# Kernel optimization log

Hardware: AMD Instinct MI355X
Metric: run time of the kernel (lower is better)

## Reference

```python
import jax, jax.numpy as jnp
import numpy as np

B, S, H = 16, 8192, 256


def setup_inputs() -> dict:
    key = jax.random.key(0)
    k1, k2, k3, k4, k5, k6 = jax.random.split(key, 6)
    # He/Glorot-ish scaling for the linear layer is irrelevant for correctness; use small randn.
    return {
        "query": jax.random.normal(k1, (B, 1, H), dtype=jnp.float32),
        "key": jax.random.normal(k2, (B, S, H), dtype=jnp.float32),
        "value": jax.random.normal(k3, (B, S, H), dtype=jnp.float32),
        "W_attn": jax.random.normal(k4, (H, 2 * H), dtype=jnp.float32) * 0.05,  # nn.Linear(2H, H).weight
        "b_attn": jax.random.normal(k5, (H,), dtype=jnp.float32) * 0.05,
        "v": jax.random.uniform(k6, (H,), dtype=jnp.float32),  # torch.rand init
    }


def reference(query, key, value, W_attn, b_attn, v):
    # Faithful to: tanh(Linear(cat([query.repeat(S), key], -1))) @ v -> softmax -> weighted sum.
    # Split the Linear weight so we never materialize the repeated/concatenated [B,S,2H] tensor:
    # cat([q,k]) @ W.T == q @ Wq.T + k @ Wk.T, with Wq = W[:, :H], Wk = W[:, H:].
    Wq = W_attn[:, :H]  # [H, H]
    Wk = W_attn[:, H:]  # [H, H]
    hidden = jnp.tanh(
        jnp.einsum("bqh,oh->bqo", query, Wq)        # [B,1,H], broadcasts over S
        + jnp.einsum("bsh,oh->bso", key, Wk)        # [B,S,H]
        + b_attn
    )  # [B,S,H]
    scores = jnp.einsum("bsh,h->bs", hidden, v)      # [B,S]
    attn_weights = jax.nn.softmax(scores, axis=-1)   # softmax over sequence
    context = jnp.einsum("bs,bsh->bh", attn_weights, value)[:, None, :]  # [B,1,H]
    return context, attn_weights
```

## Files before the change

kernel.cpp:

```cpp
#include <hip/hip_runtime.h>

#define B_SZ 16
#define S_SZ 8192
#define H_SZ 256

typedef _Float16 half8 __attribute__((ext_vector_type(8)));
typedef float f32x4 __attribute__((ext_vector_type(4)));

__device__ __forceinline__ float tanh_fast(float x) {
  float e = __expf(2.0f * x);
  return 1.0f - 2.0f / (e + 1.0f);
}

__global__ __launch_bounds__(256) void prep_kernel(
    const float* __restrict__ query, const float* __restrict__ W_attn,
    const float* __restrict__ b_attn, float* __restrict__ qb) {
  const int b = blockIdx.x;
  const int jo = blockIdx.y;
  const int wid = threadIdx.x >> 6;
  const int lane = threadIdx.x & 63;
  const float4 q4 = *(const float4*)(query + b * H_SZ + lane * 4);
#pragma unroll 4
  for (int i = 0; i < 16; i++) {
    const int o = jo * 64 + wid * 16 + i;
    const float4 w = *(const float4*)(W_attn + (size_t)o * 512 + lane * 4);
    float p = q4.x * w.x + q4.y * w.y + q4.z * w.z + q4.w * w.w;
#pragma unroll
    for (int off = 32; off >= 1; off >>= 1) p += __shfl_xor(p, off, 64);
    if (lane == 0) qb[b * H_SZ + o] = p + b_attn[o];
  }
}

__global__ __launch_bounds__(1024, 4) void fused_kernel(
    const float* __restrict__ key, const float* __restrict__ value,
    const float* __restrict__ W_attn, const float* __restrict__ qb,
    const float* __restrict__ vvec, float* __restrict__ scores,
    float* __restrict__ ctxp, float* __restrict__ mblk,
    float* __restrict__ zblk) {
  __shared__ _Float16 kbuf[2][32 * 256];
  __shared__ float psum[2][32];
  __shared__ float warr[32];
  __shared__ float msh;
  __shared__ float zsh;
  __shared__ float ssh;
  __shared__ float4 comb[16][64];

  const int tid = threadIdx.x;
  const int wid = tid >> 6;
  const int lane = tid & 63;
  const int n = lane & 15;
  const int quad = lane >> 4;
  const int rowBase = blockIdx.x * 256;
  const int b = rowBase >> 13;

  half8 afrag[8];
  {
    const float* wrow = W_attn + (size_t)(wid * 16 + n) * 512 + 256 + quad * 8;
#pragma unroll
    for (int ks = 0; ks < 8; ks++) {
      float4 f0 = *(const float4*)(wrow + ks * 32);
      float4 f1 = *(const float4*)(wrow + ks * 32 + 4);
      half8 a;
      a[0] = (_Float16)f0.x; a[1] = (_Float16)f0.y;
      a[2] = (_Float16)f0.z; a[3] = (_Float16)f0.w;
      a[4] = (_Float16)f1.x; a[5] = (_Float16)f1.y;
      a[6] = (_Float16)f1.z; a[7] = (_Float16)f1.w;
      afrag[ks] = a;
    }
  }
  float qbv[4], vvv[4];
#pragma unroll
  for (int rg = 0; rg < 4; rg++) {
    qbv[rg] = qb[b * H_SZ + wid * 16 + quad * 4 + rg];
    vvv[rg] = vvec[wid * 16 + quad * 4 + rg];
  }

  if (tid < 64) ((float*)psum)[tid] = 0.f;
  if (tid == 0) {
    msh = -1e30f;
    zsh = 0.f;
  }

  const int srow = tid >> 5;
  const int sseg = tid & 31;
  const size_t sbase = (size_t)(rowBase + srow) * H_SZ + sseg * 8;
  const int sdst = srow * 256 + ((sseg ^ srow) << 3);

  const float* vbase = value + (size_t)(rowBase + 2 * wid) * H_SZ + lane * 4;

  {
    float4 f0 = *(const float4*)(key + sbase);
    float4 f1 = *(const float4*)(key + sbase + 4);
    half8 h;
    h[0] = (_Float16)f0.x; h[1] = (_Float16)f0.y;
    h[2] = (_Float16)f0.z; h[3] = (_Float16)f0.w;
    h[4] = (_Float16)f1.x; h[5] = (_Float16)f1.y;
    h[6] = (_Float16)f1.z; h[7] = (_Float16)f1.w;
    *(half8*)&kbuf[0][sdst] = h;
  }
  __syncthreads();

  float4 acc4 = {0.f, 0.f, 0.f, 0.f};

  for (int c = 0; c < 8; c++) {
    const float4 va = *(const float4*)(vbase + (size_t)c * 32 * H_SZ);
    const float4 vb = *(const float4*)(vbase + (size_t)c * 32 * H_SZ + H_SZ);
    float4 g0, g1;
    if (c < 7) {
      const size_t nb = sbase + (size_t)(c + 1) * 32 * H_SZ;
      g0 = *(const float4*)(key + nb);
      g1 = *(const float4*)(key + nb + 4);
    }
    const _Float16* kb = kbuf[c & 1];
#pragma unroll
    for (int rt = 0; rt < 2; rt++) {
      const int lrow = rt * 16 + n;
      f32x4 acc = {0.f, 0.f, 0.f, 0.f};
#pragma unroll
      for (int ks = 0; ks < 8; ks++) {
        half8 bfrag =
            *(const half8*)&kb[lrow * 256 + (((ks * 4 + quad) ^ lrow) << 3)];
        acc = __builtin_amdgcn_mfma_f32_16x16x32_f16(afrag[ks], bfrag, acc,
                                                     0, 0, 0);
      }
      float p = 0.f;
#pragma unroll
      for (int rg = 0; rg < 4; rg++)
        p = fmaf(vvv[rg], tanh_fast(qbv[rg] + acc[rg]), p);
      p += __shfl_xor(p, 16, 64);
      p += __shfl_xor(p, 32, 64);
      if (quad == 0) atomicAdd(&psum[c & 1][lrow], p);
    }
    if (c < 7) {
      half8 h;
      h[0] = (_Float16)g0.x; h[1] = (_Float16)g0.y;
      h[2] = (_Float16)g0.z; h[3] = (_Float16)g0.w;
      h[4] = (_Float16)g1.x; h[5] = (_Float16)g1.y;
      h[6] = (_Float16)g1.z; h[7] = (_Float16)g1.w;
      *(half8*)&kbuf[(c + 1) & 1][sdst] = h;
    }
    __syncthreads();

    if (wid == 0) {
      float s = (lane < 32) ? psum[c & 1][lane] : -1e30f;
      if (lane < 32) {
        scores[rowBase + c * 32 + lane] = s;
        psum[c & 1][lane] = 0.f;
      }
      float cm = s;
#pragma unroll
      for (int off = 32; off >= 1; off >>= 1)
        cm = fmaxf(cm, __shfl_xor(cm, off, 64));
      const float m_old = msh;
      const float m_new = fmaxf(m_old, cm);
      const float scl = __expf(m_old - m_new);
      float w = (lane < 32) ? __expf(s - m_new) : 0.f;
      if (lane < 32) warr[lane] = w;
      float zc = w;
#pragma unroll
      for (int off = 32; off >= 1; off >>= 1) zc += __shfl_xor(zc, off, 64);
      if (lane == 0) {
        msh = m_new;
        zsh = fmaf(zsh, scl, zc);
        ssh = scl;
      }
    }
    __syncthreads();

    const float scl = ssh;
    const float w0 = warr[2 * wid];
    const float w1 = warr[2 * wid + 1];
    acc4.x = fmaf(w1, vb.x, fmaf(w0, va.x, acc4.x * scl));
    acc4.y = fmaf(w1, vb.y, fmaf(w0, va.y, acc4.y * scl));
    acc4.z = fmaf(w1, vb.z, fmaf(w0, va.z, acc4.z * scl));
    acc4.w = fmaf(w1, vb.w, fmaf(w0, va.w, acc4.w * scl));
  }

  comb[wid][lane] = acc4;
  __syncthreads();
  if (tid < 64) {
    float4 t4 = comb[0][tid];
#pragma unroll
    for (int j = 1; j < 16; j++) {
      const float4 u = comb[j][tid];
      t4.x += u.x; t4.y += u.y; t4.z += u.z; t4.w += u.w;
    }
    *(float4*)(ctxp + (size_t)blockIdx.x * 256 + tid * 4) = t4;
  }
  if (tid == 0) {
    mblk[blockIdx.x] = msh;
    zblk[blockIdx.x] = zsh;
  }
}

__global__ __launch_bounds__(1024) void combine_kernel(
    const float* __restrict__ ctxp, const float* __restrict__ mblk,
    const float* __restrict__ zblk, float* __restrict__ attn,
    float* __restrict__ ctx) {
  const int b = blockIdx.x;
  const int t = threadIdx.x;
  __shared__ float ms[32], zs[32];
  if (t < 32) {
    ms[t] = mblk[b * 32 + t];
    zs[t] = zblk[b * 32 + t];
  }
  __syncthreads();
  float m = -1e30f;
#pragma unroll
  for (int j = 0; j < 32; j++) m = fmaxf(m, ms[j]);
  float Z = 0.f;
  float e[32];
#pragma unroll
  for (int j = 0; j < 32; j++) {
    e[j] = __expf(ms[j] - m);
    Z = fmaf(zs[j], e[j], Z);
  }
  const float invZ = 1.0f / Z;
  if (t < 256) {
    float acc = 0.f;
#pragma unroll
    for (int j = 0; j < 32; j++)
      acc = fmaf(ctxp[(size_t)(b * 32 + j) * 256 + t], e[j], acc);
    ctx[b * H_SZ + t] = acc * invZ;
  }
  float* arow = attn + (size_t)b * S_SZ;
#pragma unroll
  for (int k = 0; k < 8; k++) {
    const int idx = k * 1024 + t;
    arow[idx] = __expf(arow[idx] - m) * invZ;
  }
}

extern "C" void kernel_launch(void* const* d_in, const int* in_sizes, int n_in,
                              void* d_out, int out_size, void* d_ws,
                              size_t ws_size, hipStream_t stream) {
  const float* query = (const float*)d_in[0];
  const float* key = (const float*)d_in[1];
  const float* value = (const float*)d_in[2];
  const float* W_attn = (const float*)d_in[3];
  const float* b_attn = (const float*)d_in[4];
  const float* vvec = (const float*)d_in[5];

  float* out = (float*)d_out;
  float* ctx = out;
  float* attn = out + 4096;
  float* ctxp = (float*)d_ws;
  float* mblk = ctxp + 512 * 256;
  float* zblk = mblk + 512;

  prep_kernel<<<dim3(B_SZ, 4), 256, 0, stream>>>(query, W_attn, b_attn, ctx);
  fused_kernel<<<512, 1024, 0, stream>>>(key, value, W_attn, ctx, vvec, attn,
                                         ctxp, mblk, zblk);
  combine_kernel<<<B_SZ, 1024, 0, stream>>>(ctxp, mblk, zblk, attn, ctx);
}
```

Baseline: 313.5 us.

## Halve block size, give each warp two output tiles, and do softmax redundantly per warp

The fused kernel now runs 512 threads per block instead of 1024. Each warp computes two 16-wide output tiles with two MFMA accumulators and reuses each B fragment read from shared memory. The online-softmax update, previously done by warp 0 and broadcast through shared memory behind a second barrier, is now computed redundantly in every warp using shuffles, which removes one __syncthreads per chunk. The psum buffer gets one slot per chunk so it never needs resetting. In exchange, each thread holds twice the A fragments and does twice the key/value loads, which raises register pressure and may reduce how many waves can be resident.

```diff
diff --git a/kernel.cpp b/kernel.cpp
--- a/kernel.cpp
+++ b/kernel.cpp
@@ -31,19 +31,15 @@
   }
 }
 
-__global__ __launch_bounds__(1024, 4) void fused_kernel(
+__global__ __launch_bounds__(512, 4) void fused_kernel(
     const float* __restrict__ key, const float* __restrict__ value,
     const float* __restrict__ W_attn, const float* __restrict__ qb,
     const float* __restrict__ vvec, float* __restrict__ scores,
     float* __restrict__ ctxp, float* __restrict__ mblk,
     float* __restrict__ zblk) {
   __shared__ _Float16 kbuf[2][32 * 256];
-  __shared__ float psum[2][32];
-  __shared__ float warr[32];
-  __shared__ float msh;
-  __shared__ float zsh;
-  __shared__ float ssh;
-  __shared__ float4 comb[16][64];
+  __shared__ float psum[8][32];
+  __shared__ float4 comb[8][64];
 
   const int tid = threadIdx.x;
   const int wid = tid >> 6;
@@ -51,11 +47,13 @@
   const int n = lane & 15;
   const int quad = lane >> 4;
   const int rowBase = blockIdx.x * 256;
-  const int b = rowBase >> 13;
-
-  half8 afrag[8];
-  {
-    const float* wrow = W_attn + (size_t)(wid * 16 + n) * 512 + 256 + quad * 8;
+  const int b = blockIdx.x >> 5;
+
+  half8 afrag[2][8];
+#pragma unroll
+  for (int ot = 0; ot < 2; ot++) {
+    const float* wrow =
+        W_attn + (size_t)((wid * 2 + ot) * 16 + n) * 512 + 256 + quad * 8;
 #pragma unroll
     for (int ks = 0; ks < 8; ks++) {
       float4 f0 = *(const float4*)(wrow + ks * 32);
@@ -65,115 +63,135 @@
       a[2] = (_Float16)f0.z; a[3] = (_Float16)f0.w;
       a[4] = (_Float16)f1.x; a[5] = (_Float16)f1.y;
       a[6] = (_Float16)f1.z; a[7] = (_Float16)f1.w;
-      afrag[ks] = a;
-    }
-  }
-  float qbv[4], vvv[4];
-#pragma unroll
-  for (int rg = 0; rg < 4; rg++) {
-    qbv[rg] = qb[b * H_SZ + wid * 16 + quad * 4 + rg];
-    vvv[rg] = vvec[wid * 16 + quad * 4 + rg];
-  }
-
-  if (tid < 64) ((float*)psum)[tid] = 0.f;
-  if (tid == 0) {
-    msh = -1e30f;
-    zsh = 0.f;
-  }
-
-  const int srow = tid >> 5;
-  const int sseg = tid & 31;
-  const size_t sbase = (size_t)(rowBase + srow) * H_SZ + sseg * 8;
-  const int sdst = srow * 256 + ((sseg ^ srow) << 3);
-
-  const float* vbase = value + (size_t)(rowBase + 2 * wid) * H_SZ + lane * 4;
+      afrag[ot][ks] = a;
+    }
+  }
+  float qbv[2][4], vvv[2][4];
+#pragma unroll
+  for (int ot = 0; ot < 2; ot++)
+#pragma unroll
+    for (int rg = 0; rg < 4; rg++) {
+      const int o = (wid * 2 + ot) * 16 + quad * 4 + rg;
+      qbv[ot][rg] = qb[b * H_SZ + o];
+      vvv[ot][rg] = vvec[o];
+    }
+
+  if (tid < 256) ((float*)psum)[tid] = 0.f;
+
+  const int srow = tid >> 4;
+  const int s0 = (tid & 15) * 2;
+  const size_t sbase = (size_t)(rowBase + srow) * H_SZ + (tid & 15) * 16;
+  const int sd0 = srow * 256 + ((s0 ^ srow) << 3);
+  const int sd1 = srow * 256 + (((s0 + 1) ^ srow) << 3);
+
+  const float* vbase = value + (size_t)(rowBase + 4 * wid) * H_SZ + lane * 4;
 
   {
     float4 f0 = *(const float4*)(key + sbase);
     float4 f1 = *(const float4*)(key + sbase + 4);
-    half8 h;
-    h[0] = (_Float16)f0.x; h[1] = (_Float16)f0.y;
-    h[2] = (_Float16)f0.z; h[3] = (_Float16)f0.w;
-    h[4] = (_Float16)f1.x; h[5] = (_Float16)f1.y;
-    h[6] = (_Float16)f1.z; h[7] = (_Float16)f1.w;
-    *(half8*)&kbuf[0][sdst] = h;
+    float4 f2 = *(const float4*)(key + sbase + 8);
+    float4 f3 = *(const float4*)(key + sbase + 12);
+    half8 h0, h1;
+    h0[0] = (_Float16)f0.x; h0[1] = (_Float16)f0.y;
+    h0[2] = (_Float16)f0.z; h0[3] = (_Float16)f0.w;
+    h0[4] = (_Float16)f1.x; h0[5] = (_Float16)f1.y;
+    h0[6] = (_Float16)f1.z; h0[7] = (_Float16)f1.w;
+    h1[0] = (_Float16)f2.x; h1[1] = (_Float16)f2.y;
+    h1[2] = (_Float16)f2.z; h1[3] = (_Float16)f2.w;
+    h1[4] = (_Float16)f3.x; h1[5] = (_Float16)f3.y;
+    h1[6] = (_Float16)f3.z; h1[7] = (_Float16)f3.w;
+    *(half8*)&kbuf[0][sd0] = h0;
+    *(half8*)&kbuf[0][sd1] = h1;
   }
   __syncthreads();
 
   float4 acc4 = {0.f, 0.f, 0.f, 0.f};
+  float m_run = -1e30f;
+  float z_run = 0.f;
 
   for (int c = 0; c < 8; c++) {
-    const float4 va = *(const float4*)(vbase + (size_t)c * 32 * H_SZ);
-    const float4 vb = *(const float4*)(vbase + (size_t)c * 32 * H_SZ + H_SZ);
-    float4 g0, g1;
+    const float4 va0 = *(const float4*)(vbase + (size_t)c * 32 * H_SZ);
+    const float4 va1 = *(const float4*)(vbase + (size_t)c * 32 * H_SZ + H_SZ);
+    const float4 va2 =
+        *(const float4*)(vbase + (size_t)c * 32 * H_SZ + 2 * H_SZ);
+    const float4 va3 =
+        *(const float4*)(vbase + (size_t)c * 32 * H_SZ + 3 * H_SZ);
+    float4 g0, g1, g2, g3;
     if (c < 7) {
       const size_t nb = sbase + (size_t)(c + 1) * 32 * H_SZ;
       g0 = *(const float4*)(key + nb);
       g1 = *(const float4*)(key + nb + 4);
+      g2 = *(const float4*)(key + nb + 8);
+      g3 = *(const float4*)(key + nb + 12);
     }
     const _Float16* kb = kbuf[c & 1];
 #pragma unroll
     for (int rt = 0; rt < 2; rt++) {
       const int lrow = rt * 16 + n;
-      f32x4 acc = {0.f, 0.f, 0.f, 0.f};
+      f32x4 acc0 = {0.f, 0.f, 0.f, 0.f};
+      f32x4 acc1 = {0.f, 0.f, 0.f, 0.f};
 #pragma unroll
       for (int ks = 0; ks < 8; ks++) {
         half8 bfrag =
             *(const half8*)&kb[lrow * 256 + (((ks * 4 + quad) ^ lrow) << 3)];
-        acc = __builtin_amdgcn_mfma_f32_16x16x32_f16(afrag[ks], bfrag, acc,
-                                                     0, 0, 0);
+        acc0 = __builtin_amdgcn_mfma_f32_16x16x32_f16(afrag[0][ks], bfrag,
+                                                      acc0, 0, 0, 0);
+        acc1 = __builtin_amdgcn_mfma_f32_16x16x32_f16(afrag[1][ks], bfrag,
+                                                      acc1, 0, 0, 0);
       }
       float p = 0.f;
 #pragma unroll
-      for (int rg = 0; rg < 4; rg++)
-        p = fmaf(vvv[rg], tanh_fast(qbv[rg] + acc[rg]), p);
+      for (int rg = 0; rg < 4; rg++) {
+        p = fmaf(vvv[0][rg], tanh_fast(qbv[0][rg] + acc0[rg]), p);
+        p = fmaf(vvv[1][rg], tanh_fast(qbv[1][rg] + acc1[rg]), p);
+      }
       p += __shfl_xor(p, 16, 64);
       p += __shfl_xor(p, 32, 64);
-      if (quad == 0) atomicAdd(&psum[c & 1][lrow], p);
+      if (quad == 0) atomicAdd(&psum[c][lrow], p);
     }
     if (c < 7) {
-      half8 h;
-      h[0] = (_Float16)g0.x; h[1] = (_Float16)g0.y;
-      h[2] = (_Float16)g0.z; h[3] = (_Float16)g0.w;
-      h[4] = (_Float16)g1.x; h[5] = (_Float16)g1.y;
-      h[6] = (_Float16)g1.z; h[7] = (_Float16)g1.w;
-      *(half8*)&kbuf[(c + 1) & 1][sdst] = h;
+      half8 h0, h1;
+      h0[0] = (_Float16)g0.x; h0[1] = (_Float16)g0.y;
+      h0[2] = (_Float16)g0.z; h0[3] = (_Float16)g0.w;
+      h0[4] = (_Float16)g1.x; h0[5] = (_Float16)g1.y;
+      h0[6] = (_Float16)g1.z; h0[7] = (_Float16)g1.w;
+      h1[0] = (_Float16)g2.x; h1[1] = (_Float16)g2.y;
+      h1[2] = (_Float16)g2.z; h1[3] = (_Float16)g2.w;
+      h1[4] = (_Float16)g3.x; h1[5] = (_Float16)g3.y;
+      h1[6] = (_Float16)g3.z; h1[7] = (_Float16)g3.w;
+      *(half8*)&kbuf[(c + 1) & 1][sd0] = h0;
+      *(half8*)&kbuf[(c + 1) & 1][sd1] = h1;
     }
     __syncthreads();
 
+    const float sv = psum[c][lane & 31];
+    float cm = sv;
+#pragma unroll
+    for (int off = 16; off >= 1; off >>= 1)
+      cm = fmaxf(cm, __shfl_xor(cm, off, 64));
+    const float m_new = fmaxf(m_run, cm);
+    const float scl = __expf(m_run - m_new);
+    m_run = m_new;
+    const float wl = __expf(sv - m_new);
     if (wid == 0) {
-      float s = (lane < 32) ? psum[c & 1][lane] : -1e30f;
-      if (lane < 32) {
-        scores[rowBase + c * 32 + lane] = s;
-        psum[c & 1][lane] = 0.f;
-      }
-      float cm = s;
-#pragma unroll
-      for (int off = 32; off >= 1; off >>= 1)
-        cm = fmaxf(cm, __shfl_xor(cm, off, 64));
-      const float m_old = msh;
-      const float m_new = fmaxf(m_old, cm);
-      const float scl = __expf(m_old - m_new);
-      float w = (lane < 32) ? __expf(s - m_new) : 0.f;
-      if (lane < 32) warr[lane] = w;
-      float zc = w;
-#pragma unroll
-      for (int off = 32; off >= 1; off >>= 1) zc += __shfl_xor(zc, off, 64);
-      if (lane == 0) {
-        msh = m_new;
-        zsh = fmaf(zsh, scl, zc);
-        ssh = scl;
-      }
-    }
-    __syncthreads();
-
-    const float scl = ssh;
-    const float w0 = warr[2 * wid];
-    const float w1 = warr[2 * wid + 1];
-    acc4.x = fmaf(w1, vb.x, fmaf(w0, va.x, acc4.x * scl));
-    acc4.y = fmaf(w1, vb.y, fmaf(w0, va.y, acc4.y * scl));
-    acc4.z = fmaf(w1, vb.z, fmaf(w0, va.z, acc4.z * scl));
-    acc4.w = fmaf(w1, vb.w, fmaf(w0, va.w, acc4.w * scl));
+      if (lane < 32) scores[rowBase + c * 32 + lane] = sv;
+      float zc = wl;
+#pragma unroll
+      for (int off = 16; off >= 1; off >>= 1) zc += __shfl_xor(zc, off, 64);
+      z_run = fmaf(z_run, scl, zc);
+    }
+    const float w0 = __shfl(wl, 4 * wid + 0, 64);
+    const float w1 = __shfl(wl, 4 * wid + 1, 64);
+    const float w2 = __shfl(wl, 4 * wid + 2, 64);
+    const float w3 = __shfl(wl, 4 * wid + 3, 64);
+    acc4.x = fmaf(w3, va3.x,
+             fmaf(w2, va2.x, fmaf(w1, va1.x, fmaf(w0, va0.x, acc4.x * scl))));
+    acc4.y = fmaf(w3, va3.y,
+             fmaf(w2, va2.y, fmaf(w1, va1.y, fmaf(w0, va0.y, acc4.y * scl))));
+    acc4.z = fmaf(w3, va3.z,
+             fmaf(w2, va2.z, fmaf(w1, va1.z, fmaf(w0, va0.z, acc4.z * scl))));
+    acc4.w = fmaf(w3, va3.w,
+             fmaf(w2, va2.w, fmaf(w1, va1.w, fmaf(w0, va0.w, acc4.w * scl))));
   }
 
   comb[wid][lane] = acc4;
@@ -181,15 +199,15 @@
   if (tid < 64) {
     float4 t4 = comb[0][tid];
 #pragma unroll
-    for (int j = 1; j < 16; j++) {
+    for (int j = 1; j < 8; j++) {
       const float4 u = comb[j][tid];
       t4.x += u.x; t4.y += u.y; t4.z += u.z; t4.w += u.w;
     }
     *(float4*)(ctxp + (size_t)blockIdx.x * 256 + tid * 4) = t4;
   }
   if (tid == 0) {
-    mblk[blockIdx.x] = msh;
-    zblk[blockIdx.x] = zsh;
+    mblk[blockIdx.x] = m_run;
+    zblk[blockIdx.x] = z_run;
   }
 }
 
@@ -249,7 +267,7 @@
   float* zblk = mblk + 512;
 
   prep_kernel<<<dim3(B_SZ, 4), 256, 0, stream>>>(query, W_attn, b_attn, ctx);
-  fused_kernel<<<512, 1024, 0, stream>>>(key, value, W_attn, ctx, vvec, attn,
-                                         ctxp, mblk, zblk);
+  fused_kernel<<<512, 512, 0, stream>>>(key, value, W_attn, ctx, vvec, attn,
+                                        ctxp, mblk, zblk);
   combine_kernel<<<B_SZ, 1024, 0, stream>>>(ctxp, mblk, zblk, attn, ctx);
 }
```

Result: slower. 396.0 us (+26.3%).
